# Performance work log

Measured on AMD Instinct MI355X. Metric: run time of the kernel, lower is better.

## Reference

```python
import jax, jax.numpy as jnp
import numpy as np

D = 1024      # total input features
R = 32        # number of ragged regions
RMAX = 32     # max region size (padding target)
HIDDEN = [128, 128]
H1, H2 = HIDDEN
B = 8192      # batch size


def _made_masks(r, rmax, hidden):
    """TFP AutoregressiveNetwork masks (left-to-right order, 'equal' hidden degrees,
    params=2, use_bias=False), zero-padded to rmax features."""
    order = np.arange(1, r + 1)
    degs = [order]
    for u in hidden:
        mn = min(int(degs[-1].min()), r - 1)
        degs.append(np.maximum(mn, np.ceil(np.arange(1, u + 1) * (r - 1) / float(u + 1)).astype(np.int64)))
    m1 = np.zeros((rmax, hidden[0]), bool)
    m1[:r] = degs[0][:, None] <= degs[1][None, :]
    m2 = degs[1][:, None] <= degs[2][None, :]
    mout = np.zeros((hidden[-1], rmax * 2), bool)
    out_deg = np.repeat(order, 2)  # output layout is feature-major: [feat, param]
    mout[:, :2 * r] = degs[-1][:, None] < out_deg[None, :]
    return m1, m2, mout


def setup_inputs() -> dict:
    rng = np.random.default_rng(0)
    perm = rng.permutation(D)
    sizes = rng.integers(8, RMAX + 1, size=R)
    idx = np.zeros((R, RMAX), np.int64)
    valid = np.zeros((R, RMAX), bool)
    M1 = np.zeros((R, RMAX, H1), bool)
    M2 = np.zeros((R, H1, H2), bool)
    Mout = np.zeros((R, H2, RMAX * 2), bool)
    pos = 0
    for i in range(R):
        s = int(sizes[i])
        idx[i, :s] = perm[pos:pos + s]
        pos += s
        valid[i, :s] = True
        M1[i], M2[i], Mout[i] = _made_masks(s, RMAX, HIDDEN)
    key = jax.random.key(0)
    k1, k2, k3, k4 = jax.random.split(key, 4)
    inputs = jax.random.normal(k1, (B, D), jnp.float32)
    W1 = jax.random.normal(k2, (R, RMAX, H1), jnp.float32) / np.float32(np.sqrt(RMAX))
    W2 = jax.random.normal(k3, (R, H1, H2), jnp.float32) / np.float32(np.sqrt(H1))
    Wout = jax.random.normal(k4, (R, H2, RMAX * 2), jnp.float32) / np.float32(np.sqrt(H2))
    return {"inputs": inputs, "W1": W1, "W2": W2, "Wout": Wout,
            "idx": jnp.asarray(idx), "valid": jnp.asarray(valid),
            "M1": jnp.asarray(M1), "M2": jnp.asarray(M2), "Mout": jnp.asarray(Mout)}


def reference(inputs, W1, W2, Wout, idx, valid, M1, M2, Mout):
    f = inputs.dtype
    v = valid.astype(f)                              # [R, RMAX]
    xg = jnp.take(inputs, idx, axis=1) * v           # [B, R, RMAX] ragged gather (padded)
    # MADE masked MLP (relu, no bias), batched over all regions at once
    h1 = jax.nn.relu(jnp.einsum('brd,rdh->brh', xg, W1 * M1.astype(f)))
    h2 = jax.nn.relu(jnp.einsum('brh,rhk->brk', h1, W2 * M2.astype(f)))
    out = jnp.einsum('brk,rko->bro', h2, Wout * Mout.astype(f))
    out = out.reshape(out.shape[0], out.shape[1], RMAX, 2)
    shift, log_s = out[..., 0], out[..., 1]
    # MAF inverse: u = (x - shift) * exp(-log_scale); logdet = -sum(log_scale)
    u = (xg - shift) * jnp.exp(-log_s)
    elem = -0.5 * u * u - 0.5 * jnp.log(2.0 * jnp.pi) - log_s
    ll = jnp.sum(elem * v, axis=-1)                  # [B, R]
    return ll[..., None]                             # [B, R, 1] as in tf.stack of expand_dims
```

## Files before the change

### kernel.cpp

```cpp
#include <hip/hip_runtime.h>
#include <math.h>


#define RR 32
#define DD 1024
#define HH 128
#define OO 64
#define TROWS 32
#define TILES_PER_BLOCK 8
#define BLOCKS_PER_R 32

#define SHP 136
#define SXG 40
#define SSC 136

typedef _Float16 f16x8_t __attribute__((ext_vector_type(8)));
typedef float f32x4_t __attribute__((ext_vector_type(4)));
typedef unsigned short u16;
typedef unsigned int u32;

__device__ __forceinline__ u16 f16b(float x) {
    _Float16 h = (_Float16)x;
    union { _Float16 f; u16 u; } c; c.f = h; return c.u;
}
__device__ __forceinline__ f32x4_t mfma16h(f16x8_t a, f16x8_t b, f32x4_t c) {
    return __builtin_amdgcn_mfma_f32_16x16x32_f16(a, b, c, 0, 0, 0);
}

__device__ __forceinline__ void stage_block16(const float* __restrict__ W,
                                              const int* __restrict__ M,
                                              int ldc, int c0, int K, u16* dst,
                                              int tid)
{
    const int kb = tid >> 3;
    const int cb = tid & 7;
    if (kb * 4 >= K) return;
    const int k0 = kb * 4;
    float e[4][4];
#pragma unroll
    for (int i = 0; i < 4; ++i) {
        const int o = ((k0 + i) * ldc + c0 + 4 * cb) >> 2;
        float4 w = ((const float4*)W)[o];
        int4   m = ((const int4*)M)[o];
        e[i][0] = m.x ? w.x : 0.f; e[i][1] = m.y ? w.y : 0.f;
        e[i][2] = m.z ? w.z : 0.f; e[i][3] = m.w ? w.w : 0.f;
    }
#pragma unroll
    for (int j = 0; j < 4; ++j) {
        ushort4 p;
        p.x = f16b(e[0][j]); p.y = f16b(e[1][j]);
        p.z = f16b(e[2][j]); p.w = f16b(e[3][j]);
        *(ushort4*)&dst[(4 * cb + j) * SSC + k0] = p;
    }
}

__device__ __forceinline__ void relu_store16(u16* __restrict__ dst, int o, f32x4_t a)
{
    ushort4 s;
    s.x = f16b(fmaxf(a[0], 0.f));
    s.y = f16b(fmaxf(a[1], 0.f));
    s.z = f16b(fmaxf(a[2], 0.f));
    s.w = f16b(fmaxf(a[3], 0.f));
    *(ushort4*)&dst[o] = s;
}

__global__ __launch_bounds__(512, 6)
void made_flow_r13(const float* __restrict__ inputs,
                   const float* __restrict__ W1,
                   const float* __restrict__ W2,
                   const float* __restrict__ Wout,
                   const int* __restrict__ idx,
                   const int* __restrict__ valid,
                   const int* __restrict__ M1,
                   const int* __restrict__ M2,
                   const int* __restrict__ Mout,
                   float* __restrict__ out)
{
    __shared__ __align__(16) u16 h1s[2][TROWS * SHP];
    __shared__ __align__(16) u16 h2s[2][TROWS * SHP];
    __shared__ __align__(16) u16 xgh[4][TROWS * SXG];
    __shared__ __align__(16) float red_all[TILES_PER_BLOCK][TROWS][4];
    __shared__ int   idx_s[RR];
    __shared__ float v_s[RR];

    u16* const scr  = h1s[0];
    u16* const scr2 = h1s[1];

    const int tid  = threadIdx.x;
    const int r    = blockIdx.x / BLOCKS_PER_R;
    const int rb   = blockIdx.x % BLOCKS_PER_R;
    const int lane = tid & 63;
    const int wave = tid >> 6;
    const int q    = lane >> 4;
    const int l16  = lane & 15;
    const int wm3  = wave & 3;
    const int ni3  = wave >> 2;

    if (tid < RR) {
        idx_s[tid] = idx[r * RR + tid];
        v_s[tid]   = valid[r * RR + tid] ? 1.f : 0.f;
    }

    f16x8_t a1;
    f16x8_t a2[4];
    f16x8_t ao[4];
    {
        const float* W1r = W1 + r * RR * HH;   const int* M1r = M1 + r * RR * HH;
        const float* W2r = W2 + r * HH * HH;   const int* M2r = M2 + r * HH * HH;
        const float* Wor = Wout + r * HH * OO; const int* Mor = Mout + r * HH * OO;
        const int c = wave >> 1, h = wave & 1;
        for (int i = 0; i < 2; ++i) {
            __syncthreads();
            if (tid < 256) stage_block16(W2r, M2r, HH, 32 * (2 * i),     HH, scr,  tid);
            else           stage_block16(W2r, M2r, HH, 32 * (2 * i + 1), HH, scr2, tid - 256);
            __syncthreads();
            if (c == 2 * i) {
#pragma unroll
                for (int ks = 0; ks < 4; ++ks)
                    a2[ks] = *(const f16x8_t*)&scr[(16 * h + l16) * SSC + ks * 32 + q * 8];
            } else if (c == 2 * i + 1) {
#pragma unroll
                for (int ks = 0; ks < 4; ++ks)
                    a2[ks] = *(const f16x8_t*)&scr2[(16 * h + l16) * SSC + ks * 32 + q * 8];
            }
        }
        {
            __syncthreads();
            if (tid < 256) stage_block16(Wor, Mor, OO, 0,  HH, scr,  tid);
            else           stage_block16(Wor, Mor, OO, 32, HH, scr2, tid - 256);
            __syncthreads();
            const u16* s = (wm3 >> 1) ? scr2 : scr;
#pragma unroll
            for (int ks = 0; ks < 4; ++ks)
                ao[ks] = *(const f16x8_t*)&s[(16 * (wm3 & 1) + l16) * SSC + ks * 32 + q * 8];
        }
        for (int i = 0; i < 2; ++i) {
            __syncthreads();
            if (tid < 256) stage_block16(W1r, M1r, HH, 32 * (2 * i),     RR, scr,  tid);
            else           stage_block16(W1r, M1r, HH, 32 * (2 * i + 1), RR, scr2, tid - 256);
            __syncthreads();
            if (c == 2 * i)          a1 = *(const f16x8_t*)&scr [(16 * h + l16) * SSC + q * 8];
            else if (c == 2 * i + 1) a1 = *(const f16x8_t*)&scr2[(16 * h + l16) * SSC + q * 8];
        }
    }
    __syncthreads();

    const f32x4_t zero4 = {0.f, 0.f, 0.f, 0.f};
    const int grow = tid >> 4;
    const int gg   = tid & 15;

    const int   ci0 = idx_s[2 * gg], ci1 = idx_s[2 * gg + 1];
    const float cv0 = v_s[2 * gg],   cv1 = v_s[2 * gg + 1];
    const int   gbase = (rb * TILES_PER_BLOCK * TROWS + grow) * DD;

    {
        float a0 = inputs[gbase + ci0] * cv0;
        float a1v = inputs[gbase + ci1] * cv1;
        float b0 = inputs[gbase + TROWS * DD + ci0] * cv0;
        float b1 = inputs[gbase + TROWS * DD + ci1] * cv1;
        *(u32*)&xgh[0][grow * SXG + 2 * gg] = (u32)f16b(a0) | ((u32)f16b(a1v) << 16);
        *(u32*)&xgh[1][grow * SXG + 2 * gg] = (u32)f16b(b0) | ((u32)f16b(b1) << 16);
    }
    __syncthreads();

    {
#pragma unroll
        for (int ni = 0; ni < 2; ++ni) {
            f16x8_t b = *(const f16x8_t*)&xgh[0][(16 * ni + l16) * SXG + q * 8];
            f32x4_t a = mfma16h(a1, b, zero4);
            relu_store16(h1s[0], (16 * ni + l16) * SHP + 16 * wave + 4 * q, a);
        }
    }

    for (int t = 0; t <= TILES_PER_BLOCK; ++t) {
        __syncthreads();

        const bool doP2  = (t < TILES_PER_BLOCK);
        const bool doP3  = (t >= 1);
        const bool doP1n = (t + 1 < TILES_PER_BLOCK);
        const bool doG   = (t + 2 < TILES_PER_BLOCK);

        float gx0, gx1;
        if (doG) {
            const int base = gbase + (t + 2) * (TROWS * DD);
            gx0 = inputs[base + ci0] * cv0;
            gx1 = inputs[base + ci1] * cv1;
        }

        f32x4_t acc3 = zero4;
        if (doP3) {
            const u16* h2b = h2s[(t - 1) & 1];
#pragma unroll
            for (int ks = 0; ks < 4; ++ks) {
                f16x8_t b = *(const f16x8_t*)&h2b[(16 * ni3 + l16) * SHP + ks * 32 + q * 8];
                acc3 = mfma16h(ao[ks], b, acc3);
            }
        }

        if (doP2) {
            const u16* h1b = h1s[t & 1];
            u16*       h2b = h2s[t & 1];
            f32x4_t acc[2] = {zero4, zero4};
#pragma unroll
            for (int ks = 0; ks < 4; ++ks) {
#pragma unroll
                for (int ni = 0; ni < 2; ++ni) {
                    f16x8_t b = *(const f16x8_t*)&h1b[(16 * ni + l16) * SHP + ks * 32 + q * 8];
                    acc[ni] = mfma16h(a2[ks], b, acc[ni]);
                }
            }
#pragma unroll
            for (int ni = 0; ni < 2; ++ni)
                relu_store16(h2b, (16 * ni + l16) * SHP + 16 * wave + 4 * q, acc[ni]);
        }

        if (doP1n) {
            const u16* xb  = xgh[(t + 1) & 3];
            u16*       h1b = h1s[(t + 1) & 1];
#pragma unroll
            for (int ni = 0; ni < 2; ++ni) {
                f16x8_t b = *(const f16x8_t*)&xb[(16 * ni + l16) * SXG + q * 8];
                f32x4_t a = mfma16h(a1, b, zero4);
                relu_store16(h1b, (16 * ni + l16) * SHP + 16 * wave + 4 * q, a);
            }
        }

        if (doP3) {
            const int j0 = 8 * wm3 + 2 * q;
            const float vj0 = v_s[j0], vj1 = v_s[j0 + 1];
            const int row = 16 * ni3 + l16;
            u32 xw = *(const u32*)&xgh[(t - 1) & 3][row * SXG + j0];
            union { u32 u; _Float16 h[2]; } xc; xc.u = xw;
            const float xv0 = (float)xc.h[0], xv1 = (float)xc.h[1];
            const float u0 = (xv0 - acc3[0]) * __expf(-acc3[1]);
            const float u1 = (xv1 - acc3[2]) * __expf(-acc3[3]);
            float p = (-0.5f * u0 * u0 - 0.91893853320467266954f - acc3[1]) * vj0
                    + (-0.5f * u1 * u1 - 0.91893853320467266954f - acc3[3]) * vj1;
            p += __shfl_xor(p, 16, 64);
            p += __shfl_xor(p, 32, 64);
            if (q == 0) red_all[t - 1][row][wm3] = p;
        }

        if (doG) {
            *(u32*)&xgh[(t + 2) & 3][grow * SXG + 2 * gg] =
                (u32)f16b(gx0) | ((u32)f16b(gx1) << 16);
        }
    }

    __syncthreads();
    if (tid < TILES_PER_BLOCK * TROWS) {
        const int tt  = tid >> 5;
        const int row = tid & 31;
        float4 rv = *(const float4*)&red_all[tt][row][0];
        out[((rb * TILES_PER_BLOCK + tt) * TROWS + row) * RR + r] =
            rv.x + rv.y + rv.z + rv.w;
    }
}

extern "C" void kernel_launch(void* const* d_in, const int* in_sizes, int n_in,
                              void* d_out, int out_size, void* d_ws, size_t ws_size,
                              hipStream_t stream)
{
    const float* inputs = (const float*)d_in[0];
    const float* W1     = (const float*)d_in[1];
    const float* W2     = (const float*)d_in[2];
    const float* Wout   = (const float*)d_in[3];
    const int*   idx    = (const int*)d_in[4];
    const int*   valid  = (const int*)d_in[5];
    const int*   M1     = (const int*)d_in[6];
    const int*   M2     = (const int*)d_in[7];
    const int*   Mout   = (const int*)d_in[8];
    float*       out    = (float*)d_out;

    hipLaunchKernelGGL(made_flow_r13, dim3(RR * BLOCKS_PER_R), dim3(512), 0, stream,
                       inputs, W1, W2, Wout, idx, valid, M1, M2, Mout, out);
}
```

Measured before the change: 125.1 us.

## Split ragged gather into a separate coalesced pre-pass kernel writing fp16 region-major xg

Adds a gather kernel that reads each input row coalesced into shared memory, applies the region permutation and validity mask, converts to fp16, and writes a region-major [R, B, 32] buffer to workspace. The main MLP kernel then reads contiguous xg tiles straight from global memory into MFMA operands instead of doing scattered per-element gathers and staging through LDS. This removes the uncoalesced random accesses and an LDS ring buffer, and raises the occupancy hint. The cost is a second launch plus an extra global write and read of the gathered buffer.

```diff
diff --git a/kernel.cpp b/kernel.cpp
--- a/kernel.cpp
+++ b/kernel.cpp
@@ -4,14 +4,15 @@
 
 #define RR 32
 #define DD 1024
+#define BB 8192
 #define HH 128
 #define OO 64
 #define TROWS 32
 #define TILES_PER_BLOCK 8
 #define BLOCKS_PER_R 32
+#define GROWS 8
 
 #define SHP 136
-#define SXG 40
 #define SSC 136
 
 typedef _Float16 f16x8_t __attribute__((ext_vector_type(8)));
@@ -25,6 +26,37 @@
 }
 __device__ __forceinline__ f32x4_t mfma16h(f16x8_t a, f16x8_t b, f32x4_t c) {
     return __builtin_amdgcn_mfma_f32_16x16x32_f16(a, b, c, 0, 0, 0);
+}
+
+__global__ __launch_bounds__(256, 8)
+void gather_xg(const float* __restrict__ inputs,
+               const int* __restrict__ idx,
+               const int* __restrict__ valid,
+               u16* __restrict__ xg)
+{
+    __shared__ float rowbuf[DD];
+    __shared__ int   idx_s[RR * 32];
+    __shared__ float v_s[RR * 32];
+    const int tid = threadIdx.x;
+    for (int i = tid; i < RR * 32; i += 256) {
+        idx_s[i] = idx[i];
+        v_s[i]   = valid[i] ? 1.f : 0.f;
+    }
+    const int b0 = blockIdx.x * GROWS;
+    const int f  = tid * 4;
+    const int r  = f >> 5, j = f & 31;
+    for (int rr = 0; rr < GROWS; ++rr) {
+        const int b = b0 + rr;
+        __syncthreads();
+        *(float4*)&rowbuf[tid * 4] = *(const float4*)&inputs[b * DD + tid * 4];
+        __syncthreads();
+        ushort4 o;
+        o.x = f16b(rowbuf[idx_s[f + 0]] * v_s[f + 0]);
+        o.y = f16b(rowbuf[idx_s[f + 1]] * v_s[f + 1]);
+        o.z = f16b(rowbuf[idx_s[f + 2]] * v_s[f + 2]);
+        o.w = f16b(rowbuf[idx_s[f + 3]] * v_s[f + 3]);
+        *(ushort4*)&xg[(size_t)r * (BB * 32) + (size_t)b * 32 + j] = o;
+    }
 }
 
 __device__ __forceinline__ void stage_block16(const float* __restrict__ W,
@@ -64,12 +96,11 @@
     *(ushort4*)&dst[o] = s;
 }
 
-__global__ __launch_bounds__(512, 6)
-void made_flow_r13(const float* __restrict__ inputs,
+__global__ __launch_bounds__(512, 8)
+void made_flow_r14(const u16* __restrict__ xg,
                    const float* __restrict__ W1,
                    const float* __restrict__ W2,
                    const float* __restrict__ Wout,
-                   const int* __restrict__ idx,
                    const int* __restrict__ valid,
                    const int* __restrict__ M1,
                    const int* __restrict__ M2,
@@ -78,9 +109,7 @@
 {
     __shared__ __align__(16) u16 h1s[2][TROWS * SHP];
     __shared__ __align__(16) u16 h2s[2][TROWS * SHP];
-    __shared__ __align__(16) u16 xgh[4][TROWS * SXG];
     __shared__ __align__(16) float red_all[TILES_PER_BLOCK][TROWS][4];
-    __shared__ int   idx_s[RR];
     __shared__ float v_s[RR];
 
     u16* const scr  = h1s[0];
@@ -96,10 +125,10 @@
     const int wm3  = wave & 3;
     const int ni3  = wave >> 2;
 
-    if (tid < RR) {
-        idx_s[tid] = idx[r * RR + tid];
-        v_s[tid]   = valid[r * RR + tid] ? 1.f : 0.f;
-    }
+    if (tid < RR) v_s[tid] = valid[r * RR + tid] ? 1.f : 0.f;
+
+    const u16* const xgp = xg + (size_t)r * (BB * 32)
+                              + (size_t)(rb * TILES_PER_BLOCK * TROWS) * 32;
 
     f16x8_t a1;
     f16x8_t a2[4];
@@ -146,27 +175,11 @@
     __syncthreads();
 
     const f32x4_t zero4 = {0.f, 0.f, 0.f, 0.f};
-    const int grow = tid >> 4;
-    const int gg   = tid & 15;
-
-    const int   ci0 = idx_s[2 * gg], ci1 = idx_s[2 * gg + 1];
-    const float cv0 = v_s[2 * gg],   cv1 = v_s[2 * gg + 1];
-    const int   gbase = (rb * TILES_PER_BLOCK * TROWS + grow) * DD;
 
     {
-        float a0 = inputs[gbase + ci0] * cv0;
-        float a1v = inputs[gbase + ci1] * cv1;
-        float b0 = inputs[gbase + TROWS * DD + ci0] * cv0;
-        float b1 = inputs[gbase + TROWS * DD + ci1] * cv1;
-        *(u32*)&xgh[0][grow * SXG + 2 * gg] = (u32)f16b(a0) | ((u32)f16b(a1v) << 16);
-        *(u32*)&xgh[1][grow * SXG + 2 * gg] = (u32)f16b(b0) | ((u32)f16b(b1) << 16);
-    }
-    __syncthreads();
-
-    {
 #pragma unroll
         for (int ni = 0; ni < 2; ++ni) {
-            f16x8_t b = *(const f16x8_t*)&xgh[0][(16 * ni + l16) * SXG + q * 8];
+            f16x8_t b = *(const f16x8_t*)&xgp[(16 * ni + l16) * 32 + q * 8];
             f32x4_t a = mfma16h(a1, b, zero4);
             relu_store16(h1s[0], (16 * ni + l16) * SHP + 16 * wave + 4 * q, a);
         }
@@ -178,14 +191,19 @@
         const bool doP2  = (t < TILES_PER_BLOCK);
         const bool doP3  = (t >= 1);
         const bool doP1n = (t + 1 < TILES_PER_BLOCK);
-        const bool doG   = (t + 2 < TILES_PER_BLOCK);
-
-        float gx0, gx1;
-        if (doG) {
-            const int base = gbase + (t + 2) * (TROWS * DD);
-            gx0 = inputs[base + ci0] * cv0;
-            gx1 = inputs[base + ci1] * cv1;
-        }
+
+        f16x8_t b1[2];
+        if (doP1n) {
+            const u16* xb = xgp + (size_t)((t + 1) * TROWS) * 32;
+#pragma unroll
+            for (int ni = 0; ni < 2; ++ni)
+                b1[ni] = *(const f16x8_t*)&xb[(16 * ni + l16) * 32 + q * 8];
+        }
+        const int j0  = 8 * wm3 + 2 * q;
+        const int row = 16 * ni3 + l16;
+        u32 xw = 0;
+        if (doP3)
+            xw = *(const u32*)&xgp[(size_t)((t - 1) * TROWS + row) * 32 + j0];
 
         f32x4_t acc3 = zero4;
         if (doP3) {
@@ -215,21 +233,16 @@
         }
 
         if (doP1n) {
-            const u16* xb  = xgh[(t + 1) & 3];
-            u16*       h1b = h1s[(t + 1) & 1];
+            u16* h1b = h1s[(t + 1) & 1];
 #pragma unroll
             for (int ni = 0; ni < 2; ++ni) {
-                f16x8_t b = *(const f16x8_t*)&xb[(16 * ni + l16) * SXG + q * 8];
-                f32x4_t a = mfma16h(a1, b, zero4);
+                f32x4_t a = mfma16h(a1, b1[ni], zero4);
                 relu_store16(h1b, (16 * ni + l16) * SHP + 16 * wave + 4 * q, a);
             }
         }
 
         if (doP3) {
-            const int j0 = 8 * wm3 + 2 * q;
             const float vj0 = v_s[j0], vj1 = v_s[j0 + 1];
-            const int row = 16 * ni3 + l16;
-            u32 xw = *(const u32*)&xgh[(t - 1) & 3][row * SXG + j0];
             union { u32 u; _Float16 h[2]; } xc; xc.u = xw;
             const float xv0 = (float)xc.h[0], xv1 = (float)xc.h[1];
             const float u0 = (xv0 - acc3[0]) * __expf(-acc3[1]);
@@ -239,11 +252,6 @@
             p += __shfl_xor(p, 16, 64);
             p += __shfl_xor(p, 32, 64);
             if (q == 0) red_all[t - 1][row][wm3] = p;
-        }
-
-        if (doG) {
-            *(u32*)&xgh[(t + 2) & 3][grow * SXG + 2 * gg] =
-                (u32)f16b(gx0) | ((u32)f16b(gx1) << 16);
         }
     }
 
@@ -271,7 +279,10 @@
     const int*   M2     = (const int*)d_in[7];
     const int*   Mout   = (const int*)d_in[8];
     float*       out    = (float*)d_out;
-
-    hipLaunchKernelGGL(made_flow_r13, dim3(RR * BLOCKS_PER_R), dim3(512), 0, stream,
-                       inputs, W1, W2, Wout, idx, valid, M1, M2, Mout, out);
-}
+    u16*         xg     = (u16*)d_ws;
+
+    hipLaunchKernelGGL(gather_xg, dim3(BB / GROWS), dim3(256), 0, stream,
+                       inputs, idx, valid, xg);
+    hipLaunchKernelGGL(made_flow_r14, dim3(RR * BLOCKS_PER_R), dim3(512), 0, stream,
+                       xg, W1, W2, Wout, valid, M1, M2, Mout, out);
+}
```

After: 162.2 us. 29.6% more time.
